# Kernel optimization log

Measured on AMD Instinct MI355X. Metric: run time of the kernel, lower is better.

The kernel has to match this reference:

```python
import jax, jax.numpy as jnp
import numpy as np

B, H, W = 8192, 5, 5
DICT, SE, CC, E, NZ = 14, 32, 64, 256, 512
EPS = 1e-4


def _conv(x, w, b):
    # x: [B,C,H,W], w: [O,C,3,3] -> SAME padding, stride 1
    y = jax.lax.conv_general_dilated(x, w, (1, 1), 'SAME',
                                     dimension_numbers=('NCHW', 'OIHW', 'NCHW'))
    return y + b[None, :, None, None]


def _embed(idx, table, cw, cb):
    emb = table[idx]                                  # [B,H,W,SE]
    # nn.Embedding(max_norm=1): renorm looked-up rows to norm <= 1
    n = jnp.sqrt(jnp.sum(emb * emb, axis=-1, keepdims=True))
    emb = emb * jnp.minimum(1.0, 1.0 / (n + 1e-7))
    x = jnp.transpose(emb, (0, 3, 1, 2))              # [B,SE,H,W]
    return _conv(x, cw, cb)                           # [B,CC,H,W]


def _phi(x, w1, b1, w2, b2, lw, lb):
    x = jax.nn.relu(_conv(x, w1, b1))
    x = jax.nn.relu(_conv(x, w2, b2))
    x = x.reshape(x.shape[0], -1)                     # [B, 32*H*W]
    x = x @ lw.T + lb                                 # [B, E]
    return x / (jnp.sqrt(jnp.sum(x * x, axis=1, keepdims=True)) + EPS)


def setup_inputs() -> dict:
    key = jax.random.key(0)
    ks = jax.random.split(key, 20)
    g = lambda k, s, sc=0.05: (jax.random.normal(k, s, jnp.float32) * sc)
    return {
        's': jax.random.randint(ks[0], (B, H, W), 0, DICT, dtype=jnp.int32),
        's_prime': jax.random.randint(ks[1], (B, H, W), 0, DICT, dtype=jnp.int32),
        'embed_table': g(ks[2], (DICT, SE), 1.0),
        'conv_embed_w': g(ks[3], (CC, SE, 3, 3)),
        'conv_embed_b': g(ks[4], (CC,)),
        'phi1_conv1_w': g(ks[5], (16, CC, 3, 3)),
        'phi1_conv1_b': g(ks[6], (16,)),
        'phi1_conv2_w': g(ks[7], (32, 16, 3, 3)),
        'phi1_conv2_b': g(ks[8], (32,)),
        'phi1_lin_w': g(ks[9], (E, H * W * 32)),
        'phi1_lin_b': g(ks[10], (E,)),
        'phi2_conv1_w': g(ks[11], (16, CC, 3, 3)),
        'phi2_conv1_b': g(ks[12], (16,)),
        'phi2_conv2_w': g(ks[13], (32, 16, 3, 3)),
        'phi2_conv2_b': g(ks[14], (32,)),
        'phi2_lin_w': g(ks[15], (E, H * W * 32)),
        'phi2_lin_b': g(ks[16], (E,)),
        'z_vectors': g(ks[17], (NZ, E), 1.0),
        'scale': jnp.ones((1,), jnp.float32),
    }


def reference(s, s_prime, embed_table, conv_embed_w, conv_embed_b,
              phi1_conv1_w, phi1_conv1_b, phi1_conv2_w, phi1_conv2_b,
              phi1_lin_w, phi1_lin_b,
              phi2_conv1_w, phi2_conv1_b, phi2_conv2_w, phi2_conv2_b,
              phi2_lin_w, phi2_lin_b, z_vectors, scale):
    xs = _embed(s, embed_table, conv_embed_w, conv_embed_b)
    xsp = _embed(s_prime, embed_table, conv_embed_w, conv_embed_b)
    embed1 = _phi(xs, phi1_conv1_w, phi1_conv1_b, phi1_conv2_w, phi1_conv2_b,
                  phi1_lin_w, phi1_lin_b)                 # [B,E]
    embed2 = _phi(xsp - xs, phi2_conv1_w, phi2_conv1_b, phi2_conv2_w,
                  phi2_conv2_b, phi2_lin_w, phi2_lin_b)   # [B,E]
    # codebook: L2-normalize (eps=0), cosine argmax, gather
    zn = z_vectors / jnp.sqrt(jnp.sum(z_vectors * z_vectors, axis=1, keepdims=True))
    z_inds = jnp.argmax(embed2 @ zn.T, axis=1)            # [B]
    z_matrix = zn[z_inds]                                 # [B,E]
    gramm = embed1 @ z_matrix.T                           # [B,B]
    return jnp.exp(scale) * gramm
```

## Files before the change

### kernel.cpp

```cpp
#include <hip/hip_runtime.h>
#include <hip/hip_bf16.h>

#define NB    8192
#define DICT  14
#define SE    32
#define CC    64
#define EDIM  256
#define NZV   512
#define C1N   16
#define C2N   32

typedef __attribute__((ext_vector_type(8))) short bf16x8;
typedef __attribute__((ext_vector_type(4))) float f32x4;

__device__ __forceinline__ void split_hl(float x, unsigned short& h, unsigned short& l) {
    unsigned u = __float_as_uint(x);
    unsigned short hh = (unsigned short)(u >> 16);
    float hf = __uint_as_float((unsigned)hh << 16);
    float lof = x - hf;
    unsigned ul = __float_as_uint(lof);
    l = (unsigned short)((ul + 0x7FFFu + ((ul >> 16) & 1u)) >> 16);
    h = hh;
}

__global__ __launch_bounds__(64) void k_norm_embed(const float* __restrict__ tab,
                                                   float* __restrict__ tn) {
    int d = blockIdx.x, l = threadIdx.x;
    float v = (l < SE) ? tab[d * SE + l] : 0.f;
    float s = v * v;
    #pragma unroll
    for (int o = 32; o > 0; o >>= 1) s += __shfl_down(s, o, 64);
    s = __shfl(s, 0, 64);
    float sc = fminf(1.f, 1.f / (sqrtf(s) + 1e-7f));
    if (l < SE) tn[d * SE + l] = v * sc;
}

__global__ __launch_bounds__(256) void k_prep_zw(const float* __restrict__ z,
        const float* __restrict__ lwa, const float* __restrict__ lwb,
        unsigned short* __restrict__ znh, unsigned short* __restrict__ znl,
        unsigned short* __restrict__ wh, unsigned short* __restrict__ wl) {
    int bid = blockIdx.x, t = threadIdx.x;
    if (bid < NZV) {
        __shared__ float red[4];
        float v = z[bid * EDIM + t];
        float s = v * v;
        #pragma unroll
        for (int o = 32; o > 0; o >>= 1) s += __shfl_down(s, o, 64);
        if ((t & 63) == 0) red[t >> 6] = s;
        __syncthreads();
        float tot = red[0] + red[1] + red[2] + red[3];
        float nv = v / sqrtf(tot);
        unsigned short h, l;
        split_hl(nv, h, l);
        znh[bid * EDIM + t] = h;
        znl[bid * EDIM + t] = l;
    } else {
        int i = (bid - NZV) * 256 + t;
        if (i < 2 * EDIM * 800) {
            float v = (i < EDIM * 800) ? lwa[i] : lwb[i - EDIM * 800];
            unsigned short h, l;
            split_hl(v, h, l);
            wh[i] = h; wl[i] = l;
        }
    }
}

__global__ __launch_bounds__(256) void k_prep_ab(const float* __restrict__ we,
        const float* __restrict__ tn,
        const float* __restrict__ w1a, const float* __restrict__ b1a,
        const float* __restrict__ w1b, const float* __restrict__ b1b,
        const float* __restrict__ be,
        float* __restrict__ A, float* __restrict__ beff) {
    if (blockIdx.x < 32) {
        int i = blockIdx.x * 256 + threadIdx.x;
        if (i >= DICT * CC * 9) return;
        int f = i % 9, c1 = (i / 9) % CC, d = i / (9 * CC);
        float acc = 0.f;
        #pragma unroll
        for (int c0 = 0; c0 < SE; c0++) acc += we[(c1 * SE + c0) * 9 + f] * tn[d * SE + c0];
        A[i] = acc;
    } else {
        int t = blockIdx.x - 32;
        const float* w1 = t ? w1b : w1a;
        const float* b1 = t ? b1b : b1a;
        for (int j = threadIdx.x; j < 400; j += blockDim.x) {
            int o = j / 25, y = (j / 5) % 5, x = j % 5;
            float acc = b1[o];
            if (t == 0) {
                for (int ey = 0; ey < 3; ey++) {
                    int py = y + ey - 1; if (py < 0 || py > 4) continue;
                    for (int ex = 0; ex < 3; ex++) {
                        int px = x + ex - 1; if (px < 0 || px > 4) continue;
                        for (int c1 = 0; c1 < CC; c1++)
                            acc += w1[((o * CC + c1) * 3 + ey) * 3 + ex] * be[c1];
                    }
                }
            }
            beff[t * 400 + j] = acc;
        }
    }
}

__global__ __launch_bounds__(256) void k_build_T(const float* __restrict__ w1a,
                                                 const float* __restrict__ w1b,
                                                 const float* __restrict__ A,
                                                 float* __restrict__ T) {
    int t = blockIdx.y;
    int qd = blockIdx.x;
    int d = qd % DICT, q = qd / DICT;
    int qy = q / 5, qx = q % 5;
    const float* w1 = t ? w1b : w1a;
    __shared__ float w1s[C1N * CC * 9];
    __shared__ float As[CC * 9];
    for (int i = threadIdx.x; i < C1N * CC * 9; i += 256) w1s[i] = w1[i];
    for (int i = threadIdx.x; i < CC * 9; i += 256) As[i] = A[d * CC * 9 + i];
    __syncthreads();
    float* Tout = T + (((size_t)t * 25 + q) * DICT + d) * 400;
    for (int j = threadIdx.x; j < 400; j += 256) {
        int o = j / 25, y = (j / 5) % 5, x = j % 5;
        float acc = 0.f;
        int py0 = max(0, max(y - 1, qy - 1)), py1 = min(4, min(y + 1, qy + 1));
        int px0 = max(0, max(x - 1, qx - 1)), px1 = min(4, min(x + 1, qx + 1));
        for (int py = py0; py <= py1; py++)
            for (int px = px0; px <= px1; px++) {
                int ey = py - y + 1, ex = px - x + 1;
                int fy = qy - py + 1, fx = qx - px + 1;
                const float* wp = &w1s[(o * CC) * 9 + (ey * 3 + ex)];
                const float* ap = &As[fy * 3 + fx];
                float pa = 0.f;
                #pragma unroll 8
                for (int c1 = 0; c1 < CC; c1++) pa += wp[c1 * 9] * ap[c1 * 9];
                acc += pa;
            }
        Tout[j] = acc;
    }
}

__global__ __launch_bounds__(256, 2) void k_phi(
    const int* __restrict__ s, const int* __restrict__ sp,
    const float* __restrict__ T, const float* __restrict__ beff,
    const float* __restrict__ w2a, const float* __restrict__ b2a,
    const float* __restrict__ w2b, const float* __restrict__ b2b,
    const unsigned short* __restrict__ wh, const unsigned short* __restrict__ wl,
    const float* __restrict__ lba, const float* __restrict__ lbb,
    const unsigned short* __restrict__ znh, const unsigned short* __restrict__ znl,
    float* __restrict__ Cm, int* __restrict__ idxout) {
    int phi = blockIdx.y;
    int b0 = blockIdx.x * 32;
    int tid = threadIdx.x;
    int wv = tid >> 6, lane = tid & 63, li = lane & 15, quad = lane >> 4;

    __shared__ __align__(16) char smem[79936];
    float* a1T          = (float*)smem;
    unsigned short* a2h = (unsigned short*)(smem + 52800);
    unsigned short* a2l = (unsigned short*)(smem + 65600);
    int* sbase1         = (int*)(smem + 52800);
    int* sbase2         = (int*)(smem + 56000);
    float* redq         = (float*)(smem + 78400);
    float* argv         = (float*)(smem + 78912);
    int*   argn         = (int*)(smem + 79424);
    unsigned short* emh = (unsigned short*)smem;
    unsigned short* eml = (unsigned short*)(smem + 16896);

    const float* Tg = T + (size_t)phi * (25 * DICT * 400);

    for (int i = tid; i < 800; i += 256) {
        int si = i / 25, q = i - si * 25;
        sbase1[i] = (q * DICT + s[(b0 + si) * 25 + q]) * 400;
        if (phi) sbase2[i] = (q * DICT + sp[(b0 + si) * 25 + q]) * 400;
    }
    __syncthreads();

    const float* be = beff + phi * 400;
    if (phi == 0) {
        for (int task = tid; task < 12800; task += 256) {
            int si = task / 400, j = task - si * 400;
            float acc = be[j];
            const int* sb = sbase1 + si * 25;
            #pragma unroll
            for (int q = 0; q < 25; q++) acc += Tg[sb[q] + j];
            a1T[j * 33 + si] = fmaxf(acc, 0.f);
        }
    } else {
        for (int task = tid; task < 12800; task += 256) {
            int si = task / 400, j = task - si * 400;
            float acc = be[j];
            const int* sb1 = sbase1 + si * 25;
            const int* sb2 = sbase2 + si * 25;
            #pragma unroll
            for (int q = 0; q < 25; q++) acc += Tg[sb2[q] + j] - Tg[sb1[q] + j];
            a1T[j * 33 + si] = fmaxf(acc, 0.f);
        }
    }
    __syncthreads();

    const float* w2 = phi ? w2b : w2a;
    const float* b2 = phi ? b2b : b2a;
    const unsigned short* Wh = wh + (size_t)phi * EDIM * 800;
    const unsigned short* Wl = wl + (size_t)phi * EDIM * 800;
    int n0w = wv * 64;
    f32x4 acc2[2][4];
    f32x4 zz = {0.f, 0.f, 0.f, 0.f};
    #pragma unroll
    for (int i = 0; i < 2; i++)
        #pragma unroll
        for (int j = 0; j < 4; j++) acc2[i][j] = zz;
    bf16x8 zfrag = {0, 0, 0, 0, 0, 0, 0, 0};

    int csi = tid >> 3, o2loc = tid & 7;
    for (int c = 0; c < 4; c++) {
        int o2 = c * 8 + o2loc;
        float cacc[25];
        float bias2 = b2[o2];
        #pragma unroll
        for (int p = 0; p < 25; p++) cacc[p] = bias2;
        for (int c1 = 0; c1 < C1N; c1++) {
            float row[25];
            #pragma unroll
            for (int p = 0; p < 25; p++) row[p] = a1T[(c1 * 25 + p) * 33 + csi];
            #pragma unroll
            for (int ky = 0; ky < 3; ky++)
            #pragma unroll
            for (int kx = 0; kx < 3; kx++) {
                float w = w2[((o2 * C1N + c1) * 3 + ky) * 3 + kx];
                #pragma unroll
                for (int y = 0; y < 5; y++) {
                    int iy = y + ky - 1; if (iy < 0 || iy > 4) continue;
                    #pragma unroll
                    for (int x = 0; x < 5; x++) {
                        int ix = x + kx - 1; if (ix < 0 || ix > 4) continue;
                        cacc[y * 5 + x] += w * row[iy * 5 + ix];
                    }
                }
            }
        }
        #pragma unroll
        for (int p = 0; p < 25; p++) {
            float v = fmaxf(cacc[p], 0.f);
            unsigned short h, l;
            split_hl(v, h, l);
            int ko = csi * 200 + o2loc * 25 + p;
            a2h[ko] = h; a2l[ko] = l;
        }
        __syncthreads();
        #pragma unroll
        for (int ks = 0; ks < 7; ks++) {
            bf16x8 ah0, al0, ah1, al1;
            if (ks < 6) {
                int ko = ks * 32 + quad * 8;
                ah0 = *(const bf16x8*)&a2h[li * 200 + ko];
                al0 = *(const bf16x8*)&a2l[li * 200 + ko];
                ah1 = *(const bf16x8*)&a2h[(16 + li) * 200 + ko];
                al1 = *(const bf16x8*)&a2l[(16 + li) * 200 + ko];
            } else {
                ah0 = zfrag; al0 = zfrag; ah1 = zfrag; al1 = zfrag;
                if (quad == 0) {
                    ah0 = *(const bf16x8*)&a2h[li * 200 + 192];
                    al0 = *(const bf16x8*)&a2l[li * 200 + 192];
                    ah1 = *(const bf16x8*)&a2h[(16 + li) * 200 + 192];
                    al1 = *(const bf16x8*)&a2l[(16 + li) * 200 + 192];
                }
            }
            int kglob = c * 200 + ks * 32 + quad * 8;
            #pragma unroll
            for (int nt = 0; nt < 4; nt++) {
                size_t wo = (size_t)(n0w + nt * 16 + li) * 800 + kglob;
                bf16x8 bh = *(const bf16x8*)(Wh + wo);
                bf16x8 bl = *(const bf16x8*)(Wl + wo);
                acc2[0][nt] = __builtin_amdgcn_mfma_f32_16x16x32_bf16(ah0, bh, acc2[0][nt], 0, 0, 0);
                acc2[0][nt] = __builtin_amdgcn_mfma_f32_16x16x32_bf16(ah0, bl, acc2[0][nt], 0, 0, 0);
                acc2[0][nt] = __builtin_amdgcn_mfma_f32_16x16x32_bf16(al0, bh, acc2[0][nt], 0, 0, 0);
                acc2[1][nt] = __builtin_amdgcn_mfma_f32_16x16x32_bf16(ah1, bh, acc2[1][nt], 0, 0, 0);
                acc2[1][nt] = __builtin_amdgcn_mfma_f32_16x16x32_bf16(ah1, bl, acc2[1][nt], 0, 0, 0);
                acc2[1][nt] = __builtin_amdgcn_mfma_f32_16x16x32_bf16(al1, bh, acc2[1][nt], 0, 0, 0);
            }
        }
        __syncthreads();
    }

    const float* lb = phi ? lbb : lba;
    float sq[2][4];
    #pragma unroll
    for (int mt = 0; mt < 2; mt++)
        #pragma unroll
        for (int r = 0; r < 4; r++) sq[mt][r] = 0.f;
    #pragma unroll
    for (int mt = 0; mt < 2; mt++)
        #pragma unroll
        for (int nt = 0; nt < 4; nt++) {
            float bsv = lb[n0w + nt * 16 + li];
            #pragma unroll
            for (int r = 0; r < 4; r++) {
                float v = acc2[mt][nt][r] + bsv;
                acc2[mt][nt][r] = v;
                sq[mt][r] += v * v;
            }
        }
    #pragma unroll
    for (int off = 1; off < 16; off <<= 1)
        #pragma unroll
        for (int mt = 0; mt < 2; mt++)
            #pragma unroll
            for (int r = 0; r < 4; r++)
                sq[mt][r] += __shfl_xor(sq[mt][r], off, 64);
    if (li == 0) {
        #pragma unroll
        for (int mt = 0; mt < 2; mt++)
            #pragma unroll
            for (int r = 0; r < 4; r++)
                redq[(mt * 16 + quad * 4 + r) * 4 + wv] = sq[mt][r];
    }
    __syncthreads();
    #pragma unroll
    for (int mt = 0; mt < 2; mt++)
        #pragma unroll
        for (int r = 0; r < 4; r++) {
            int rowm = mt * 16 + quad * 4 + r;
            float tot = redq[rowm * 4 + 0] + redq[rowm * 4 + 1] +
                        redq[rowm * 4 + 2] + redq[rowm * 4 + 3];
            float inv = 1.f / (sqrtf(tot) + 1e-4f);
            #pragma unroll
            for (int nt = 0; nt < 4; nt++) {
                float v = acc2[mt][nt][r] * inv;
                unsigned short h, l;
                split_hl(v, h, l);
                int col = n0w + nt * 16 + li;
                emh[rowm * 264 + col] = h;
                eml[rowm * 264 + col] = l;
            }
        }
    __syncthreads();

    f32x4 acc3[2][8];
    #pragma unroll
    for (int i = 0; i < 2; i++)
        #pragma unroll
        for (int j = 0; j < 8; j++) acc3[i][j] = zz;
    int zn0 = wv * 128;
    #pragma unroll
    for (int ks = 0; ks < 8; ks++) {
        int ko = ks * 32 + quad * 8;
        bf16x8 ah0 = *(const bf16x8*)&emh[li * 264 + ko];
        bf16x8 al0 = *(const bf16x8*)&eml[li * 264 + ko];
        bf16x8 ah1 = *(const bf16x8*)&emh[(16 + li) * 264 + ko];
        bf16x8 al1 = *(const bf16x8*)&eml[(16 + li) * 264 + ko];
        #pragma unroll
        for (int nt = 0; nt < 8; nt++) {
            size_t zo = (size_t)(zn0 + nt * 16 + li) * EDIM + ko;
            bf16x8 bh = *(const bf16x8*)(znh + zo);
            bf16x8 bl = *(const bf16x8*)(znl + zo);
            acc3[0][nt] = __builtin_amdgcn_mfma_f32_16x16x32_bf16(ah0, bh, acc3[0][nt], 0, 0, 0);
            acc3[0][nt] = __builtin_amdgcn_mfma_f32_16x16x32_bf16(ah0, bl, acc3[0][nt], 0, 0, 0);
            acc3[0][nt] = __builtin_amdgcn_mfma_f32_16x16x32_bf16(al0, bh, acc3[0][nt], 0, 0, 0);
            acc3[1][nt] = __builtin_amdgcn_mfma_f32_16x16x32_bf16(ah1, bh, acc3[1][nt], 0, 0, 0);
            acc3[1][nt] = __builtin_amdgcn_mfma_f32_16x16x32_bf16(ah1, bl, acc3[1][nt], 0, 0, 0);
            acc3[1][nt] = __builtin_amdgcn_mfma_f32_16x16x32_bf16(al1, bh, acc3[1][nt], 0, 0, 0);
        }
    }

    if (phi == 0) {
        #pragma unroll
        for (int mt = 0; mt < 2; mt++)
            #pragma unroll
            for (int nt = 0; nt < 8; nt++)
                #pragma unroll
                for (int r = 0; r < 4; r++)
                    Cm[(size_t)(b0 + mt * 16 + quad * 4 + r) * NZV + zn0 + nt * 16 + li] =
                        acc3[mt][nt][r];
    } else {
        #pragma unroll
        for (int mt = 0; mt < 2; mt++)
            #pragma unroll
            for (int r = 0; r < 4; r++) {
                float best = -3.0e38f; int bn = 0;
                #pragma unroll
                for (int nt = 0; nt < 8; nt++) {
                    float v = acc3[mt][nt][r];
                    int n = zn0 + nt * 16 + li;
                    if (v > best) { best = v; bn = n; }
                }
                #pragma unroll
                for (int off = 1; off < 16; off <<= 1) {
                    float ov = __shfl_xor(best, off, 64);
                    int   on = __shfl_xor(bn, off, 64);
                    if (ov > best || (ov == best && on < bn)) { best = ov; bn = on; }
                }
                if (li == 0) {
                    int rowm = mt * 16 + quad * 4 + r;
                    argv[rowm * 4 + wv] = best;
                    argn[rowm * 4 + wv] = bn;
                }
            }
        __syncthreads();
        if (tid < 32) {
            float best = argv[tid * 4]; int bn = argn[tid * 4];
            #pragma unroll
            for (int w = 1; w < 4; w++) {
                float v = argv[tid * 4 + w]; int n = argn[tid * 4 + w];
                if (v > best || (v == best && n < bn)) { best = v; bn = n; }
            }
            idxout[b0 + tid] = bn;
        }
    }
}

__global__ __launch_bounds__(256) void k_out(const float* __restrict__ C,
                                             const int* __restrict__ idx,
                                             const float* __restrict__ scale,
                                             float* __restrict__ out) {
    __shared__ float g[8][NZV];
    __shared__ int   id[2048];
    int i0 = blockIdx.y * 8;
    int j0 = blockIdx.x * 2048;
    float esc = expf(scale[0]);
    for (int u = threadIdx.x; u < 2048; u += 256) id[u] = idx[j0 + u];
    for (int u = threadIdx.x; u < 8 * NZV; u += 256) {
        int r = u >> 9, c = u & 511;
        g[r][c] = C[(size_t)(i0 + r) * NZV + c];
    }
    __syncthreads();
    int jb = threadIdx.x * 8;
    int myid[8];
    #pragma unroll
    for (int u = 0; u < 8; u++) myid[u] = id[jb + u];
    #pragma unroll
    for (int r = 0; r < 8; r++) {
        float4 o0, o1;
        o0.x = esc * g[r][myid[0]]; o0.y = esc * g[r][myid[1]];
        o0.z = esc * g[r][myid[2]]; o0.w = esc * g[r][myid[3]];
        o1.x = esc * g[r][myid[4]]; o1.y = esc * g[r][myid[5]];
        o1.z = esc * g[r][myid[6]]; o1.w = esc * g[r][myid[7]];
        float4* dst = (float4*)(out + (size_t)(i0 + r) * NB + j0 + jb);
        dst[0] = o0; dst[1] = o1;
    }
}

extern "C" void kernel_launch(void* const* d_in, const int* in_sizes, int n_in,
                              void* d_out, int out_size, void* d_ws, size_t ws_size,
                              hipStream_t stream) {
    const int*   s     = (const int*)d_in[0];
    const int*   sp    = (const int*)d_in[1];
    const float* tab   = (const float*)d_in[2];
    const float* wE    = (const float*)d_in[3];
    const float* bE    = (const float*)d_in[4];
    const float* w1a   = (const float*)d_in[5];
    const float* b1a   = (const float*)d_in[6];
    const float* w2a   = (const float*)d_in[7];
    const float* b2a   = (const float*)d_in[8];
    const float* lwa   = (const float*)d_in[9];
    const float* lba   = (const float*)d_in[10];
    const float* w1b   = (const float*)d_in[11];
    const float* b1b   = (const float*)d_in[12];
    const float* w2b   = (const float*)d_in[13];
    const float* b2b   = (const float*)d_in[14];
    const float* lwb   = (const float*)d_in[15];
    const float* lbb   = (const float*)d_in[16];
    const float* zv    = (const float*)d_in[17];
    const float* scale = (const float*)d_in[18];

    float* out = (float*)d_out;
    float* wsf = (float*)d_ws;

    float* tn   = wsf;
    float* Aw   = wsf + 448;
    float* beff = wsf + 8512;
    int*   idx  = (int*)(wsf + 9312);
    float* T    = wsf + 17504;
    float* Cm   = wsf + 297504;
    unsigned short* wh  = (unsigned short*)(wsf + 4491808);
    unsigned short* wl  = (unsigned short*)(wsf + 4696608);
    unsigned short* znh = (unsigned short*)(wsf + 4901408);
    unsigned short* znl = (unsigned short*)(wsf + 4966944);

    k_norm_embed<<<DICT, 64, 0, stream>>>(tab, tn);
    k_prep_zw<<<NZV + 1600, 256, 0, stream>>>(zv, lwa, lwb, znh, znl, wh, wl);
    k_prep_ab<<<34, 256, 0, stream>>>(wE, tn, w1a, b1a, w1b, b1b, bE, Aw, beff);
    k_build_T<<<dim3(25 * DICT, 2), 256, 0, stream>>>(w1a, w1b, Aw, T);
    k_phi<<<dim3(NB / 32, 2), 256, 0, stream>>>(s, sp, T, beff, w2a, b2a, w2b, b2b,
                                                wh, wl, lba, lbb, znh, znl, Cm, idx);
    k_out<<<dim3(NB / 2048, NB / 8), 256, 0, stream>>>(Cm, idx, scale, out);
}
```

Before: 531.0 us.

## Halve k_phi batch tile, split conv2 pixels across waves, vectorize T gather

Cuts the per-block sample tile in k_phi from 32 to 16, shrinking shared memory and raising launch bounds to 4 blocks per CU. Conv2 work is split so each wave computes a subset of output pixels via a templated body, which lowers per-thread register pressure. The T-table gather now uses float4 loads into a padded row-major a1 layout, and the MFMA stages run on a single 16-row M tile. In exchange, each loaded weight fragment from global memory is reused over half as many rows, so weight traffic per sample doubles, and there are more barriers per sample.

```diff
diff --git a/kernel.cpp b/kernel.cpp
--- a/kernel.cpp
+++ b/kernel.cpp
@@ -136,7 +136,51 @@
     }
 }
 
-__global__ __launch_bounds__(256, 2) void k_phi(
+template<int P0, int P1>
+__device__ __forceinline__ void conv2_body(const float* __restrict__ a1row,
+                                           const float* __restrict__ w2,
+                                           int o2, float bias2,
+                                           unsigned short* __restrict__ a2h,
+                                           unsigned short* __restrict__ a2l,
+                                           int kbase) {
+    constexpr int NP = P1 - P0;
+    float cacc[NP];
+    #pragma unroll
+    for (int i = 0; i < NP; i++) cacc[i] = bias2;
+    for (int c1 = 0; c1 < C1N; c1++) {
+        const float* rp = a1row + c1 * 28;
+        float row[25];
+        #pragma unroll
+        for (int v = 0; v < 6; v++) *(float4*)&row[v * 4] = *(const float4*)&rp[v * 4];
+        row[24] = rp[24];
+        const float* wp = &w2[(o2 * C1N + c1) * 9];
+        #pragma unroll
+        for (int ky = 0; ky < 3; ky++)
+        #pragma unroll
+        for (int kx = 0; kx < 3; kx++) {
+            float w = wp[ky * 3 + kx];
+            #pragma unroll
+            for (int i = 0; i < NP; i++) {
+                constexpr_int:;
+                int p = P0 + i;
+                int y = p / 5, x = p % 5;
+                int iy = y + ky - 1, ix = x + kx - 1;
+                if (iy < 0 || iy > 4 || ix < 0 || ix > 4) continue;
+                cacc[i] += w * row[iy * 5 + ix];
+            }
+        }
+    }
+    #pragma unroll
+    for (int i = 0; i < NP; i++) {
+        float v = fmaxf(cacc[i], 0.f);
+        unsigned short h, l;
+        split_hl(v, h, l);
+        a2h[kbase + P0 + i] = h;
+        a2l[kbase + P0 + i] = l;
+    }
+}
+
+__global__ __launch_bounds__(256, 4) void k_phi(
     const int* __restrict__ s, const int* __restrict__ sp,
     const float* __restrict__ T, const float* __restrict__ beff,
     const float* __restrict__ w2a, const float* __restrict__ b2a,
@@ -146,25 +190,25 @@
     const unsigned short* __restrict__ znh, const unsigned short* __restrict__ znl,
     float* __restrict__ Cm, int* __restrict__ idxout) {
     int phi = blockIdx.y;
-    int b0 = blockIdx.x * 32;
+    int b0 = blockIdx.x * 16;
     int tid = threadIdx.x;
     int wv = tid >> 6, lane = tid & 63, li = lane & 15, quad = lane >> 4;
 
-    __shared__ __align__(16) char smem[79936];
-    float* a1T          = (float*)smem;
-    unsigned short* a2h = (unsigned short*)(smem + 52800);
-    unsigned short* a2l = (unsigned short*)(smem + 65600);
-    int* sbase1         = (int*)(smem + 52800);
-    int* sbase2         = (int*)(smem + 56000);
-    float* redq         = (float*)(smem + 78400);
-    float* argv         = (float*)(smem + 78912);
-    int*   argn         = (int*)(smem + 79424);
+    __shared__ __align__(16) char smem[37376];
+    float* a1s          = (float*)smem;
+    unsigned short* a2h = (unsigned short*)(smem + 28928);
+    unsigned short* a2l = (unsigned short*)(smem + 32768);
+    int* sbase1         = (int*)(smem + 28928);
+    int* sbase2         = (int*)(smem + 30528);
+    float* redq         = (float*)(smem + 36608);
+    float* argv         = (float*)(smem + 36864);
+    int*   argn         = (int*)(smem + 37120);
     unsigned short* emh = (unsigned short*)smem;
-    unsigned short* eml = (unsigned short*)(smem + 16896);
+    unsigned short* eml = (unsigned short*)(smem + 8448);
 
     const float* Tg = T + (size_t)phi * (25 * DICT * 400);
 
-    for (int i = tid; i < 800; i += 256) {
+    for (int i = tid; i < 400; i += 256) {
         int si = i / 25, q = i - si * 25;
         sbase1[i] = (q * DICT + s[(b0 + si) * 25 + q]) * 400;
         if (phi) sbase2[i] = (q * DICT + sp[(b0 + si) * 25 + q]) * 400;
@@ -172,24 +216,35 @@
     __syncthreads();
 
     const float* be = beff + phi * 400;
-    if (phi == 0) {
-        for (int task = tid; task < 12800; task += 256) {
-            int si = task / 400, j = task - si * 400;
-            float acc = be[j];
+    for (int task = tid; task < 1600; task += 256) {
+        int si = task / 100, t4 = task - si * 100;
+        int j = t4 * 4;
+        float4 bv = *(const float4*)&be[j];
+        float a0 = bv.x, a1v = bv.y, a2v = bv.z, a3v = bv.w;
+        if (phi == 0) {
             const int* sb = sbase1 + si * 25;
             #pragma unroll
-            for (int q = 0; q < 25; q++) acc += Tg[sb[q] + j];
-            a1T[j * 33 + si] = fmaxf(acc, 0.f);
-        }
-    } else {
-        for (int task = tid; task < 12800; task += 256) {
-            int si = task / 400, j = task - si * 400;
-            float acc = be[j];
+            for (int q = 0; q < 25; q++) {
+                float4 t = *(const float4*)&Tg[sb[q] + j];
+                a0 += t.x; a1v += t.y; a2v += t.z; a3v += t.w;
+            }
+        } else {
             const int* sb1 = sbase1 + si * 25;
             const int* sb2 = sbase2 + si * 25;
             #pragma unroll
-            for (int q = 0; q < 25; q++) acc += Tg[sb2[q] + j] - Tg[sb1[q] + j];
-            a1T[j * 33 + si] = fmaxf(acc, 0.f);
+            for (int q = 0; q < 25; q++) {
+                float4 t2 = *(const float4*)&Tg[sb2[q] + j];
+                float4 t1 = *(const float4*)&Tg[sb1[q] + j];
+                a0 += t2.x - t1.x; a1v += t2.y - t1.y;
+                a2v += t2.z - t1.z; a3v += t2.w - t1.w;
+            }
+        }
+        float vals[4] = {a0, a1v, a2v, a3v};
+        #pragma unroll
+        for (int e = 0; e < 4; e++) {
+            int jj = j + e;
+            int c1 = jj / 25, p = jj - c1 * 25;
+            a1s[si * 452 + c1 * 28 + p] = fmaxf(vals[e], 0.f);
         }
     }
     __syncthreads();
@@ -199,200 +254,156 @@
     const unsigned short* Wh = wh + (size_t)phi * EDIM * 800;
     const unsigned short* Wl = wl + (size_t)phi * EDIM * 800;
     int n0w = wv * 64;
-    f32x4 acc2[2][4];
+    f32x4 acc2[4];
     f32x4 zz = {0.f, 0.f, 0.f, 0.f};
     #pragma unroll
-    for (int i = 0; i < 2; i++)
-        #pragma unroll
-        for (int j = 0; j < 4; j++) acc2[i][j] = zz;
+    for (int j = 0; j < 4; j++) acc2[j] = zz;
     bf16x8 zfrag = {0, 0, 0, 0, 0, 0, 0, 0};
 
-    int csi = tid >> 3, o2loc = tid & 7;
-    for (int c = 0; c < 4; c++) {
-        int o2 = c * 8 + o2loc;
-        float cacc[25];
+    int csi = lane >> 2, o2loc = lane & 3;
+    const float* a1row = &a1s[csi * 452];
+    for (int c = 0; c < 8; c++) {
+        int o2 = c * 4 + o2loc;
         float bias2 = b2[o2];
-        #pragma unroll
-        for (int p = 0; p < 25; p++) cacc[p] = bias2;
-        for (int c1 = 0; c1 < C1N; c1++) {
-            float row[25];
-            #pragma unroll
-            for (int p = 0; p < 25; p++) row[p] = a1T[(c1 * 25 + p) * 33 + csi];
-            #pragma unroll
-            for (int ky = 0; ky < 3; ky++)
-            #pragma unroll
-            for (int kx = 0; kx < 3; kx++) {
-                float w = w2[((o2 * C1N + c1) * 3 + ky) * 3 + kx];
-                #pragma unroll
-                for (int y = 0; y < 5; y++) {
-                    int iy = y + ky - 1; if (iy < 0 || iy > 4) continue;
-                    #pragma unroll
-                    for (int x = 0; x < 5; x++) {
-                        int ix = x + kx - 1; if (ix < 0 || ix > 4) continue;
-                        cacc[y * 5 + x] += w * row[iy * 5 + ix];
+        int kbase = csi * 120 + o2loc * 25;
+        if (wv == 0)      conv2_body<0, 7>(a1row, w2, o2, bias2, a2h, a2l, kbase);
+        else if (wv == 1) conv2_body<7, 13>(a1row, w2, o2, bias2, a2h, a2l, kbase);
+        else if (wv == 2) conv2_body<13, 19>(a1row, w2, o2, bias2, a2h, a2l, kbase);
+        else              conv2_body<19, 25>(a1row, w2, o2, bias2, a2h, a2l, kbase);
+        __syncthreads();
+        #pragma unroll
+        for (int ks = 0; ks < 4; ks++) {
+            bf16x8 ah, al;
+            if (ks < 3) {
+                int ko = ks * 32 + quad * 8;
+                ah = *(const bf16x8*)&a2h[li * 120 + ko];
+                al = *(const bf16x8*)&a2l[li * 120 + ko];
+            } else {
+                ah = zfrag; al = zfrag;
+                if (quad == 0) {
+                    ushort4 v = *(const ushort4*)&a2h[li * 120 + 96];
+                    ah[0] = (short)v.x; ah[1] = (short)v.y; ah[2] = (short)v.z; ah[3] = (short)v.w;
+                    ushort4 u = *(const ushort4*)&a2l[li * 120 + 96];
+                    al[0] = (short)u.x; al[1] = (short)u.y; al[2] = (short)u.z; al[3] = (short)u.w;
+                }
+            }
+            #pragma unroll
+            for (int nt = 0; nt < 4; nt++) {
+                size_t nrow = (size_t)(n0w + nt * 16 + li) * 800;
+                bf16x8 bh, bl;
+                if (ks < 3) {
+                    size_t wo = nrow + c * 100 + ks * 32 + quad * 8;
+                    bh = *(const bf16x8*)(Wh + wo);
+                    bl = *(const bf16x8*)(Wl + wo);
+                } else {
+                    bh = zfrag; bl = zfrag;
+                    if (quad == 0) {
+                        size_t wo = nrow + c * 100 + 96;
+                        ushort4 v = *(const ushort4*)(Wh + wo);
+                        bh[0] = (short)v.x; bh[1] = (short)v.y; bh[2] = (short)v.z; bh[3] = (short)v.w;
+                        ushort4 u = *(const ushort4*)(Wl + wo);
+                        bl[0] = (short)u.x; bl[1] = (short)u.y; bl[2] = (short)u.z; bl[3] = (short)u.w;
                     }
                 }
-            }
-        }
-        #pragma unroll
-        for (int p = 0; p < 25; p++) {
-            float v = fmaxf(cacc[p], 0.f);
+                acc2[nt] = __builtin_amdgcn_mfma_f32_16x16x32_bf16(ah, bh, acc2[nt], 0, 0, 0);
+                acc2[nt] = __builtin_amdgcn_mfma_f32_16x16x32_bf16(ah, bl, acc2[nt], 0, 0, 0);
+                acc2[nt] = __builtin_amdgcn_mfma_f32_16x16x32_bf16(al, bh, acc2[nt], 0, 0, 0);
+            }
+        }
+        __syncthreads();
+    }
+
+    const float* lb = phi ? lbb : lba;
+    float sq[4] = {0.f, 0.f, 0.f, 0.f};
+    #pragma unroll
+    for (int nt = 0; nt < 4; nt++) {
+        float bsv = lb[n0w + nt * 16 + li];
+        #pragma unroll
+        for (int r = 0; r < 4; r++) {
+            float v = acc2[nt][r] + bsv;
+            acc2[nt][r] = v;
+            sq[r] += v * v;
+        }
+    }
+    #pragma unroll
+    for (int off = 1; off < 16; off <<= 1)
+        #pragma unroll
+        for (int r = 0; r < 4; r++)
+            sq[r] += __shfl_xor(sq[r], off, 64);
+    if (li == 0) {
+        #pragma unroll
+        for (int r = 0; r < 4; r++)
+            redq[(quad * 4 + r) * 4 + wv] = sq[r];
+    }
+    __syncthreads();
+    #pragma unroll
+    for (int r = 0; r < 4; r++) {
+        int rowm = quad * 4 + r;
+        float tot = redq[rowm * 4 + 0] + redq[rowm * 4 + 1] +
+                    redq[rowm * 4 + 2] + redq[rowm * 4 + 3];
+        float inv = 1.f / (sqrtf(tot) + 1e-4f);
+        #pragma unroll
+        for (int nt = 0; nt < 4; nt++) {
+            float v = acc2[nt][r] * inv;
             unsigned short h, l;
             split_hl(v, h, l);
-            int ko = csi * 200 + o2loc * 25 + p;
-            a2h[ko] = h; a2l[ko] = l;
-        }
-        __syncthreads();
-        #pragma unroll
-        for (int ks = 0; ks < 7; ks++) {
-            bf16x8 ah0, al0, ah1, al1;
-            if (ks < 6) {
-                int ko = ks * 32 + quad * 8;
-                ah0 = *(const bf16x8*)&a2h[li * 200 + ko];
-                al0 = *(const bf16x8*)&a2l[li * 200 + ko];
-                ah1 = *(const bf16x8*)&a2h[(16 + li) * 200 + ko];
-                al1 = *(const bf16x8*)&a2l[(16 + li) * 200 + ko];
-            } else {
-                ah0 = zfrag; al0 = zfrag; ah1 = zfrag; al1 = zfrag;
-                if (quad == 0) {
-                    ah0 = *(const bf16x8*)&a2h[li * 200 + 192];
-                    al0 = *(const bf16x8*)&a2l[li * 200 + 192];
-                    ah1 = *(const bf16x8*)&a2h[(16 + li) * 200 + 192];
-                    al1 = *(const bf16x8*)&a2l[(16 + li) * 200 + 192];
-                }
-            }
-            int kglob = c * 200 + ks * 32 + quad * 8;
-            #pragma unroll
-            for (int nt = 0; nt < 4; nt++) {
-                size_t wo = (size_t)(n0w + nt * 16 + li) * 800 + kglob;
-                bf16x8 bh = *(const bf16x8*)(Wh + wo);
-                bf16x8 bl = *(const bf16x8*)(Wl + wo);
-                acc2[0][nt] = __builtin_amdgcn_mfma_f32_16x16x32_bf16(ah0, bh, acc2[0][nt], 0, 0, 0);
-                acc2[0][nt] = __builtin_amdgcn_mfma_f32_16x16x32_bf16(ah0, bl, acc2[0][nt], 0, 0, 0);
-                acc2[0][nt] = __builtin_amdgcn_mfma_f32_16x16x32_bf16(al0, bh, acc2[0][nt], 0, 0, 0);
-                acc2[1][nt] = __builtin_amdgcn_mfma_f32_16x16x32_bf16(ah1, bh, acc2[1][nt], 0, 0, 0);
-                acc2[1][nt] = __builtin_amdgcn_mfma_f32_16x16x32_bf16(ah1, bl, acc2[1][nt], 0, 0, 0);
-                acc2[1][nt] = __builtin_amdgcn_mfma_f32_16x16x32_bf16(al1, bh, acc2[1][nt], 0, 0, 0);
-            }
-        }
-        __syncthreads();
-    }
-
-    const float* lb = phi ? lbb : lba;
-    float sq[2][4];
-    #pragma unroll
-    for (int mt = 0; mt < 2; mt++)
-        #pragma unroll
-        for (int r = 0; r < 4; r++) sq[mt][r] = 0.f;
-    #pragma unroll
-    for (int mt = 0; mt < 2; mt++)
-        #pragma unroll
-        for (int nt = 0; nt < 4; nt++) {
-            float bsv = lb[n0w + nt * 16 + li];
-            #pragma unroll
-            for (int r = 0; r < 4; r++) {
-                float v = acc2[mt][nt][r] + bsv;
-                acc2[mt][nt][r] = v;
-                sq[mt][r] += v * v;
-            }
-        }
-    #pragma unroll
-    for (int off = 1; off < 16; off <<= 1)
-        #pragma unroll
-        for (int mt = 0; mt < 2; mt++)
-            #pragma unroll
-            for (int r = 0; r < 4; r++)
-                sq[mt][r] += __shfl_xor(sq[mt][r], off, 64);
-    if (li == 0) {
-        #pragma unroll
-        for (int mt = 0; mt < 2; mt++)
-            #pragma unroll
-            for (int r = 0; r < 4; r++)
-                redq[(mt * 16 + quad * 4 + r) * 4 + wv] = sq[mt][r];
-    }
-    __syncthreads();
-    #pragma unroll
-    for (int mt = 0; mt < 2; mt++)
-        #pragma unroll
-        for (int r = 0; r < 4; r++) {
-            int rowm = mt * 16 + quad * 4 + r;
-            float tot = redq[rowm * 4 + 0] + redq[rowm * 4 + 1] +
-                        redq[rowm * 4 + 2] + redq[rowm * 4 + 3];
-            float inv = 1.f / (sqrtf(tot) + 1e-4f);
-            #pragma unroll
-            for (int nt = 0; nt < 4; nt++) {
-                float v = acc2[mt][nt][r] * inv;
-                unsigned short h, l;
-                split_hl(v, h, l);
-                int col = n0w + nt * 16 + li;
-                emh[rowm * 264 + col] = h;
-                eml[rowm * 264 + col] = l;
-            }
-        }
-    __syncthreads();
-
-    f32x4 acc3[2][8];
-    #pragma unroll
-    for (int i = 0; i < 2; i++)
-        #pragma unroll
-        for (int j = 0; j < 8; j++) acc3[i][j] = zz;
+            int col = n0w + nt * 16 + li;
+            emh[rowm * 264 + col] = h;
+            eml[rowm * 264 + col] = l;
+        }
+    }
+    __syncthreads();
+
+    f32x4 acc3[8];
+    #pragma unroll
+    for (int j = 0; j < 8; j++) acc3[j] = zz;
     int zn0 = wv * 128;
     #pragma unroll
     for (int ks = 0; ks < 8; ks++) {
         int ko = ks * 32 + quad * 8;
-        bf16x8 ah0 = *(const bf16x8*)&emh[li * 264 + ko];
-        bf16x8 al0 = *(const bf16x8*)&eml[li * 264 + ko];
-        bf16x8 ah1 = *(const bf16x8*)&emh[(16 + li) * 264 + ko];
-        bf16x8 al1 = *(const bf16x8*)&eml[(16 + li) * 264 + ko];
+        bf16x8 ah = *(const bf16x8*)&emh[li * 264 + ko];
+        bf16x8 al = *(const bf16x8*)&eml[li * 264 + ko];
         #pragma unroll
         for (int nt = 0; nt < 8; nt++) {
             size_t zo = (size_t)(zn0 + nt * 16 + li) * EDIM + ko;
             bf16x8 bh = *(const bf16x8*)(znh + zo);
             bf16x8 bl = *(const bf16x8*)(znl + zo);
-            acc3[0][nt] = __builtin_amdgcn_mfma_f32_16x16x32_bf16(ah0, bh, acc3[0][nt], 0, 0, 0);
-            acc3[0][nt] = __builtin_amdgcn_mfma_f32_16x16x32_bf16(ah0, bl, acc3[0][nt], 0, 0, 0);
-            acc3[0][nt] = __builtin_amdgcn_mfma_f32_16x16x32_bf16(al0, bh, acc3[0][nt], 0, 0, 0);
-            acc3[1][nt] = __builtin_amdgcn_mfma_f32_16x16x32_bf16(ah1, bh, acc3[1][nt], 0, 0, 0);
-            acc3[1][nt] = __builtin_amdgcn_mfma_f32_16x16x32_bf16(ah1, bl, acc3[1][nt], 0, 0, 0);
-            acc3[1][nt] = __builtin_amdgcn_mfma_f32_16x16x32_bf16(al1, bh, acc3[1][nt], 0, 0, 0);
+            acc3[nt] = __builtin_amdgcn_mfma_f32_16x16x32_bf16(ah, bh, acc3[nt], 0, 0, 0);
+            acc3[nt] = __builtin_amdgcn_mfma_f32_16x16x32_bf16(ah, bl, acc3[nt], 0, 0, 0);
+            acc3[nt] = __builtin_amdgcn_mfma_f32_16x16x32_bf16(al, bh, acc3[nt], 0, 0, 0);
         }
     }
 
     if (phi == 0) {
         #pragma unroll
-        for (int mt = 0; mt < 2; mt++)
-            #pragma unroll
-            for (int nt = 0; nt < 8; nt++)
-                #pragma unroll
-                for (int r = 0; r < 4; r++)
-                    Cm[(size_t)(b0 + mt * 16 + quad * 4 + r) * NZV + zn0 + nt * 16 + li] =
-                        acc3[mt][nt][r];
+        for (int nt = 0; nt < 8; nt++)
+            #pragma unroll
+            for (int r = 0; r < 4; r++)
+                Cm[(size_t)(b0 + quad * 4 + r) * NZV + zn0 + nt * 16 + li] = acc3[nt][r];
     } else {
         #pragma unroll
-        for (int mt = 0; mt < 2; mt++)
-            #pragma unroll
-            for (int r = 0; r < 4; r++) {
-                float best = -3.0e38f; int bn = 0;
-                #pragma unroll
-                for (int nt = 0; nt < 8; nt++) {
-                    float v = acc3[mt][nt][r];
-                    int n = zn0 + nt * 16 + li;
-                    if (v > best) { best = v; bn = n; }
-                }
-                #pragma unroll
-                for (int off = 1; off < 16; off <<= 1) {
-                    float ov = __shfl_xor(best, off, 64);
-                    int   on = __shfl_xor(bn, off, 64);
-                    if (ov > best || (ov == best && on < bn)) { best = ov; bn = on; }
-                }
-                if (li == 0) {
-                    int rowm = mt * 16 + quad * 4 + r;
-                    argv[rowm * 4 + wv] = best;
-                    argn[rowm * 4 + wv] = bn;
-                }
-            }
+        for (int r = 0; r < 4; r++) {
+            float best = -3.0e38f; int bn = 0;
+            #pragma unroll
+            for (int nt = 0; nt < 8; nt++) {
+                float v = acc3[nt][r];
+                int n = zn0 + nt * 16 + li;
+                if (v > best) { best = v; bn = n; }
+            }
+            #pragma unroll
+            for (int off = 1; off < 16; off <<= 1) {
+                float ov = __shfl_xor(best, off, 64);
+                int   on = __shfl_xor(bn, off, 64);
+                if (ov > best || (ov == best && on < bn)) { best = ov; bn = on; }
+            }
+            if (li == 0) {
+                int rowm = quad * 4 + r;
+                argv[rowm * 4 + wv] = best;
+                argn[rowm * 4 + wv] = bn;
+            }
+        }
         __syncthreads();
-        if (tid < 32) {
+        if (tid < 16) {
             float best = argv[tid * 4]; int bn = argn[tid * 4];
             #pragma unroll
             for (int w = 1; w < 4; w++) {
@@ -476,7 +487,7 @@
     k_prep_zw<<<NZV + 1600, 256, 0, stream>>>(zv, lwa, lwb, znh, znl, wh, wl);
     k_prep_ab<<<34, 256, 0, stream>>>(wE, tn, w1a, b1a, w1b, b1b, bE, Aw, beff);
     k_build_T<<<dim3(25 * DICT, 2), 256, 0, stream>>>(w1a, w1b, Aw, T);
-    k_phi<<<dim3(NB / 32, 2), 256, 0, stream>>>(s, sp, T, beff, w2a, b2a, w2b, b2b,
+    k_phi<<<dim3(NB / 16, 2), 256, 0, stream>>>(s, sp, T, beff, w2a, b2a, w2b, b2b,
                                                 wh, wl, lba, lbb, znh, znl, Cm, idx);
     k_out<<<dim3(NB / 2048, NB / 8), 256, 0, stream>>>(Cm, idx, scale, out);
 }
```

Result: slower. 673.2 us (+26.8%).

## Split fused phi kernel into conv kernel and MFMA linear/codebook kernel

Applied to the files above, without the earlier changes.

The monolithic k_phi kernel is split in two. k_gcv computes the conv1 table gather and conv2 with 16 samples per block, smaller shared memory, float4 gathers and occupancy 4. Its bf16 hi/lo activations go to a scratch buffer placed in the output array. k_emb then runs the linear MFMA GEMM straight from global memory without per-chunk syncs, followed by the codebook stage. This aims to raise occupancy and remove the syncs that serialized conv2 with the MFMA work, at the cost of an extra global round trip of the activations.

```diff
diff --git a/kernel.cpp b/kernel.cpp
--- a/kernel.cpp
+++ b/kernel.cpp
@@ -136,35 +136,22 @@
     }
 }
 
-__global__ __launch_bounds__(256, 2) void k_phi(
+__global__ __launch_bounds__(256, 4) void k_gcv(
     const int* __restrict__ s, const int* __restrict__ sp,
     const float* __restrict__ T, const float* __restrict__ beff,
     const float* __restrict__ w2a, const float* __restrict__ b2a,
     const float* __restrict__ w2b, const float* __restrict__ b2b,
-    const unsigned short* __restrict__ wh, const unsigned short* __restrict__ wl,
-    const float* __restrict__ lba, const float* __restrict__ lbb,
-    const unsigned short* __restrict__ znh, const unsigned short* __restrict__ znl,
-    float* __restrict__ Cm, int* __restrict__ idxout) {
+    unsigned short* __restrict__ a2h, unsigned short* __restrict__ a2l) {
     int phi = blockIdx.y;
-    int b0 = blockIdx.x * 32;
+    int b0 = blockIdx.x * 16;
     int tid = threadIdx.x;
-    int wv = tid >> 6, lane = tid & 63, li = lane & 15, quad = lane >> 4;
-
-    __shared__ __align__(16) char smem[79936];
-    float* a1T          = (float*)smem;
-    unsigned short* a2h = (unsigned short*)(smem + 52800);
-    unsigned short* a2l = (unsigned short*)(smem + 65600);
-    int* sbase1         = (int*)(smem + 52800);
-    int* sbase2         = (int*)(smem + 56000);
-    float* redq         = (float*)(smem + 78400);
-    float* argv         = (float*)(smem + 78912);
-    int*   argn         = (int*)(smem + 79424);
-    unsigned short* emh = (unsigned short*)smem;
-    unsigned short* eml = (unsigned short*)(smem + 16896);
+
+    __shared__ int sbase1[400], sbase2[400];
+    __shared__ __align__(16) float a1s[16 * 452];
 
     const float* Tg = T + (size_t)phi * (25 * DICT * 400);
 
-    for (int i = tid; i < 800; i += 256) {
+    for (int i = tid; i < 400; i += 256) {
         int si = i / 25, q = i - si * 25;
         sbase1[i] = (q * DICT + s[(b0 + si) * 25 + q]) * 400;
         if (phi) sbase2[i] = (q * DICT + sp[(b0 + si) * 25 + q]) * 400;
@@ -172,57 +159,62 @@
     __syncthreads();
 
     const float* be = beff + phi * 400;
-    if (phi == 0) {
-        for (int task = tid; task < 12800; task += 256) {
-            int si = task / 400, j = task - si * 400;
-            float acc = be[j];
+    for (int task = tid; task < 1600; task += 256) {
+        int si = task / 100, t4 = task - si * 100;
+        int j = t4 * 4;
+        float4 bv = *(const float4*)&be[j];
+        float a0 = bv.x, a1v = bv.y, a2v = bv.z, a3v = bv.w;
+        if (phi == 0) {
             const int* sb = sbase1 + si * 25;
             #pragma unroll
-            for (int q = 0; q < 25; q++) acc += Tg[sb[q] + j];
-            a1T[j * 33 + si] = fmaxf(acc, 0.f);
-        }
-    } else {
-        for (int task = tid; task < 12800; task += 256) {
-            int si = task / 400, j = task - si * 400;
-            float acc = be[j];
+            for (int q = 0; q < 25; q++) {
+                float4 t = *(const float4*)&Tg[sb[q] + j];
+                a0 += t.x; a1v += t.y; a2v += t.z; a3v += t.w;
+            }
+        } else {
             const int* sb1 = sbase1 + si * 25;
             const int* sb2 = sbase2 + si * 25;
             #pragma unroll
-            for (int q = 0; q < 25; q++) acc += Tg[sb2[q] + j] - Tg[sb1[q] + j];
-            a1T[j * 33 + si] = fmaxf(acc, 0.f);
+            for (int q = 0; q < 25; q++) {
+                float4 t2 = *(const float4*)&Tg[sb2[q] + j];
+                float4 t1 = *(const float4*)&Tg[sb1[q] + j];
+                a0 += t2.x - t1.x; a1v += t2.y - t1.y;
+                a2v += t2.z - t1.z; a3v += t2.w - t1.w;
+            }
+        }
+        float vals[4] = {a0, a1v, a2v, a3v};
+        #pragma unroll
+        for (int e = 0; e < 4; e++) {
+            int jj = j + e;
+            int c1 = jj / 25, p = jj - c1 * 25;
+            a1s[si * 452 + c1 * 28 + p] = fmaxf(vals[e], 0.f);
         }
     }
     __syncthreads();
 
     const float* w2 = phi ? w2b : w2a;
     const float* b2 = phi ? b2b : b2a;
-    const unsigned short* Wh = wh + (size_t)phi * EDIM * 800;
-    const unsigned short* Wl = wl + (size_t)phi * EDIM * 800;
-    int n0w = wv * 64;
-    f32x4 acc2[2][4];
-    f32x4 zz = {0.f, 0.f, 0.f, 0.f};
-    #pragma unroll
-    for (int i = 0; i < 2; i++)
-        #pragma unroll
-        for (int j = 0; j < 4; j++) acc2[i][j] = zz;
-    bf16x8 zfrag = {0, 0, 0, 0, 0, 0, 0, 0};
-
-    int csi = tid >> 3, o2loc = tid & 7;
-    for (int c = 0; c < 4; c++) {
-        int o2 = c * 8 + o2loc;
+    int csi = tid >> 4, oh = tid & 15;
+    const float* a1row = &a1s[csi * 452];
+    size_t obase = ((size_t)phi * NB + b0 + csi) * 800;
+    for (int t2 = 0; t2 < 2; t2++) {
+        int o2 = oh * 2 + t2;
         float cacc[25];
         float bias2 = b2[o2];
         #pragma unroll
         for (int p = 0; p < 25; p++) cacc[p] = bias2;
         for (int c1 = 0; c1 < C1N; c1++) {
+            const float* rp = a1row + c1 * 28;
             float row[25];
             #pragma unroll
-            for (int p = 0; p < 25; p++) row[p] = a1T[(c1 * 25 + p) * 33 + csi];
+            for (int v = 0; v < 6; v++) *(float4*)&row[v * 4] = *(const float4*)&rp[v * 4];
+            row[24] = rp[24];
+            const float* wp = &w2[(o2 * C1N + c1) * 9];
             #pragma unroll
             for (int ky = 0; ky < 3; ky++)
             #pragma unroll
             for (int kx = 0; kx < 3; kx++) {
-                float w = w2[((o2 * C1N + c1) * 3 + ky) * 3 + kx];
+                float w = wp[ky * 3 + kx];
                 #pragma unroll
                 for (int y = 0; y < 5; y++) {
                     int iy = y + ky - 1; if (iy < 0 || iy > 4) continue;
@@ -234,48 +226,65 @@
                 }
             }
         }
+        size_t kb = obase + o2 * 25;
         #pragma unroll
         for (int p = 0; p < 25; p++) {
             float v = fmaxf(cacc[p], 0.f);
             unsigned short h, l;
             split_hl(v, h, l);
-            int ko = csi * 200 + o2loc * 25 + p;
-            a2h[ko] = h; a2l[ko] = l;
-        }
-        __syncthreads();
-        #pragma unroll
-        for (int ks = 0; ks < 7; ks++) {
-            bf16x8 ah0, al0, ah1, al1;
-            if (ks < 6) {
-                int ko = ks * 32 + quad * 8;
-                ah0 = *(const bf16x8*)&a2h[li * 200 + ko];
-                al0 = *(const bf16x8*)&a2l[li * 200 + ko];
-                ah1 = *(const bf16x8*)&a2h[(16 + li) * 200 + ko];
-                al1 = *(const bf16x8*)&a2l[(16 + li) * 200 + ko];
-            } else {
-                ah0 = zfrag; al0 = zfrag; ah1 = zfrag; al1 = zfrag;
-                if (quad == 0) {
-                    ah0 = *(const bf16x8*)&a2h[li * 200 + 192];
-                    al0 = *(const bf16x8*)&a2l[li * 200 + 192];
-                    ah1 = *(const bf16x8*)&a2h[(16 + li) * 200 + 192];
-                    al1 = *(const bf16x8*)&a2l[(16 + li) * 200 + 192];
-                }
-            }
-            int kglob = c * 200 + ks * 32 + quad * 8;
-            #pragma unroll
-            for (int nt = 0; nt < 4; nt++) {
-                size_t wo = (size_t)(n0w + nt * 16 + li) * 800 + kglob;
-                bf16x8 bh = *(const bf16x8*)(Wh + wo);
-                bf16x8 bl = *(const bf16x8*)(Wl + wo);
-                acc2[0][nt] = __builtin_amdgcn_mfma_f32_16x16x32_bf16(ah0, bh, acc2[0][nt], 0, 0, 0);
-                acc2[0][nt] = __builtin_amdgcn_mfma_f32_16x16x32_bf16(ah0, bl, acc2[0][nt], 0, 0, 0);
-                acc2[0][nt] = __builtin_amdgcn_mfma_f32_16x16x32_bf16(al0, bh, acc2[0][nt], 0, 0, 0);
-                acc2[1][nt] = __builtin_amdgcn_mfma_f32_16x16x32_bf16(ah1, bh, acc2[1][nt], 0, 0, 0);
-                acc2[1][nt] = __builtin_amdgcn_mfma_f32_16x16x32_bf16(ah1, bl, acc2[1][nt], 0, 0, 0);
-                acc2[1][nt] = __builtin_amdgcn_mfma_f32_16x16x32_bf16(al1, bh, acc2[1][nt], 0, 0, 0);
-            }
-        }
-        __syncthreads();
+            a2h[kb + p] = h;
+            a2l[kb + p] = l;
+        }
+    }
+}
+
+__global__ __launch_bounds__(256) void k_emb(
+    const unsigned short* __restrict__ a2h, const unsigned short* __restrict__ a2l,
+    const unsigned short* __restrict__ wh, const unsigned short* __restrict__ wl,
+    const float* __restrict__ lba, const float* __restrict__ lbb,
+    const unsigned short* __restrict__ znh, const unsigned short* __restrict__ znl,
+    float* __restrict__ Cm, int* __restrict__ idxout) {
+    int phi = blockIdx.y;
+    int b0 = blockIdx.x * 32;
+    int tid = threadIdx.x;
+    int wv = tid >> 6, lane = tid & 63, li = lane & 15, quad = lane >> 4;
+
+    __shared__ __align__(16) unsigned short emh[32 * 264], eml[32 * 264];
+    __shared__ float redq[32 * 4];
+    __shared__ float argv[32 * 4];
+    __shared__ int   argn[32 * 4];
+
+    const unsigned short* Ah = a2h + ((size_t)phi * NB + b0) * 800;
+    const unsigned short* Al = a2l + ((size_t)phi * NB + b0) * 800;
+    const unsigned short* Wh = wh + (size_t)phi * EDIM * 800;
+    const unsigned short* Wl = wl + (size_t)phi * EDIM * 800;
+    int n0w = wv * 64;
+
+    f32x4 zz = {0.f, 0.f, 0.f, 0.f};
+    f32x4 acc2[2][4];
+    #pragma unroll
+    for (int i = 0; i < 2; i++)
+        #pragma unroll
+        for (int j = 0; j < 4; j++) acc2[i][j] = zz;
+
+    for (int k0 = 0; k0 < 800; k0 += 32) {
+        int ko = k0 + quad * 8;
+        bf16x8 ah0 = *(const bf16x8*)(Ah + (size_t)li * 800 + ko);
+        bf16x8 al0 = *(const bf16x8*)(Al + (size_t)li * 800 + ko);
+        bf16x8 ah1 = *(const bf16x8*)(Ah + (size_t)(16 + li) * 800 + ko);
+        bf16x8 al1 = *(const bf16x8*)(Al + (size_t)(16 + li) * 800 + ko);
+        #pragma unroll
+        for (int nt = 0; nt < 4; nt++) {
+            size_t wo = (size_t)(n0w + nt * 16 + li) * 800 + ko;
+            bf16x8 bh = *(const bf16x8*)(Wh + wo);
+            bf16x8 bl = *(const bf16x8*)(Wl + wo);
+            acc2[0][nt] = __builtin_amdgcn_mfma_f32_16x16x32_bf16(ah0, bh, acc2[0][nt], 0, 0, 0);
+            acc2[0][nt] = __builtin_amdgcn_mfma_f32_16x16x32_bf16(ah0, bl, acc2[0][nt], 0, 0, 0);
+            acc2[0][nt] = __builtin_amdgcn_mfma_f32_16x16x32_bf16(al0, bh, acc2[0][nt], 0, 0, 0);
+            acc2[1][nt] = __builtin_amdgcn_mfma_f32_16x16x32_bf16(ah1, bh, acc2[1][nt], 0, 0, 0);
+            acc2[1][nt] = __builtin_amdgcn_mfma_f32_16x16x32_bf16(ah1, bl, acc2[1][nt], 0, 0, 0);
+            acc2[1][nt] = __builtin_amdgcn_mfma_f32_16x16x32_bf16(al1, bh, acc2[1][nt], 0, 0, 0);
+        }
     }
 
     const float* lb = phi ? lbb : lba;
@@ -368,38 +377,46 @@
                     Cm[(size_t)(b0 + mt * 16 + quad * 4 + r) * NZV + zn0 + nt * 16 + li] =
                         acc3[mt][nt][r];
     } else {
+        float bestr[2][4] = {{-3.0e38f, -3.0e38f, -3.0e38f, -3.0e38f},
+                             {-3.0e38f, -3.0e38f, -3.0e38f, -3.0e38f}};
+        int bnr[2][4] = {{0, 0, 0, 0}, {0, 0, 0, 0}};
+        #pragma unroll
+        for (int nt = 0; nt < 8; nt++) {
+            int n = zn0 + nt * 16 + li;
+            #pragma unroll
+            for (int mt = 0; mt < 2; mt++)
+                #pragma unroll
+                for (int r = 0; r < 4; r++) {
+                    float v = acc3[mt][nt][r];
+                    if (v > bestr[mt][r]) { bestr[mt][r] = v; bnr[mt][r] = n; }
+                }
+        }
         #pragma unroll
         for (int mt = 0; mt < 2; mt++)
             #pragma unroll
             for (int r = 0; r < 4; r++) {
-                float best = -3.0e38f; int bn = 0;
-                #pragma unroll
-                for (int nt = 0; nt < 8; nt++) {
-                    float v = acc3[mt][nt][r];
-                    int n = zn0 + nt * 16 + li;
-                    if (v > best) { best = v; bn = n; }
-                }
+                float bv = bestr[mt][r]; int nv = bnr[mt][r];
                 #pragma unroll
                 for (int off = 1; off < 16; off <<= 1) {
-                    float ov = __shfl_xor(best, off, 64);
-                    int   on = __shfl_xor(bn, off, 64);
-                    if (ov > best || (ov == best && on < bn)) { best = ov; bn = on; }
+                    float ov = __shfl_xor(bv, off, 64);
+                    int   on = __shfl_xor(nv, off, 64);
+                    if (ov > bv || (ov == bv && on < nv)) { bv = ov; nv = on; }
                 }
                 if (li == 0) {
                     int rowm = mt * 16 + quad * 4 + r;
-                    argv[rowm * 4 + wv] = best;
-                    argn[rowm * 4 + wv] = bn;
+                    argv[rowm * 4 + wv] = bv;
+                    argn[rowm * 4 + wv] = nv;
                 }
             }
         __syncthreads();
         if (tid < 32) {
-            float best = argv[tid * 4]; int bn = argn[tid * 4];
+            float bv = argv[tid * 4]; int nv = argn[tid * 4];
             #pragma unroll
             for (int w = 1; w < 4; w++) {
                 float v = argv[tid * 4 + w]; int n = argn[tid * 4 + w];
-                if (v > best || (v == best && n < bn)) { best = v; bn = n; }
-            }
-            idxout[b0 + tid] = bn;
+                if (v > bv || (v == bv && n < nv)) { bv = v; nv = n; }
+            }
+            idxout[b0 + tid] = nv;
         }
     }
 }
@@ -472,11 +489,16 @@
     unsigned short* znh = (unsigned short*)(wsf + 4901408);
     unsigned short* znl = (unsigned short*)(wsf + 4966944);
 
+    unsigned short* a2h = (unsigned short*)out;
+    unsigned short* a2l = (unsigned short*)(out + 6553600);
+
     k_norm_embed<<<DICT, 64, 0, stream>>>(tab, tn);
     k_prep_zw<<<NZV + 1600, 256, 0, stream>>>(zv, lwa, lwb, znh, znl, wh, wl);
     k_prep_ab<<<34, 256, 0, stream>>>(wE, tn, w1a, b1a, w1b, b1b, bE, Aw, beff);
     k_build_T<<<dim3(25 * DICT, 2), 256, 0, stream>>>(w1a, w1b, Aw, T);
-    k_phi<<<dim3(NB / 32, 2), 256, 0, stream>>>(s, sp, T, beff, w2a, b2a, w2b, b2b,
-                                                wh, wl, lba, lbb, znh, znl, Cm, idx);
+    k_gcv<<<dim3(NB / 16, 2), 256, 0, stream>>>(s, sp, T, beff, w2a, b2a, w2b, b2b,
+                                                a2h, a2l);
+    k_emb<<<dim3(NB / 32, 2), 256, 0, stream>>>(a2h, a2l, wh, wl, lba, lbb,
+                                                znh, znl, Cm, idx);
     k_out<<<dim3(NB / 2048, NB / 8), 256, 0, stream>>>(Cm, idx, scale, out);
 }
```

Result: slower. 558.0 us (+5.1%).
